# Kernel optimization log

Hardware: AMD Instinct MI355X
Metric: run time of the kernel (lower is better)

Reference implementation:

```python
import jax, jax.numpy as jnp
import numpy as np

B, S, DIM, H = 2, 2048, 2048, 16
HD = DIM // H  # 128
ROPE_THETA = 10000.0
NEG = -1e9


def setup_inputs() -> dict:
    key = jax.random.key(0)
    ks = jax.random.split(key, 6)
    x = jax.random.normal(ks[0], (B, S, DIM), dtype=jnp.float32)
    # rotary embedding tables: angle[s, j] = s / theta^(2j/HD), j in [0, HD/2)
    inv_freq = 1.0 / (ROPE_THETA ** (jnp.arange(0, HD, 2, dtype=jnp.float32) / HD))
    angles = jnp.arange(S, dtype=jnp.float32)[:, None] * inv_freq[None, :]  # (S, HD/2)
    freqs_cos = jnp.cos(angles)
    freqs_sin = jnp.sin(angles)
    # causal additive mask (1,1,S,S)
    causal = jnp.tril(jnp.ones((S, S), dtype=jnp.bool_))
    mask = jnp.where(causal, 0.0, NEG).astype(jnp.float32)[None, None]
    sc = 1.0 / np.sqrt(DIM)
    wq = jax.random.normal(ks[1], (DIM, DIM), dtype=jnp.float32) * sc
    wk = jax.random.normal(ks[2], (DIM, DIM), dtype=jnp.float32) * sc
    wv = jax.random.normal(ks[3], (DIM, DIM), dtype=jnp.float32) * sc
    wo = jax.random.normal(ks[4], (DIM, DIM), dtype=jnp.float32) * sc
    return {"x": x, "freqs_cos": freqs_cos, "freqs_sin": freqs_sin,
            "mask": mask, "wq": wq, "wk": wk, "wv": wv, "wo": wo}


def _apply_rope(t, cos, sin):
    # t: (B,S,H,HD); cos/sin: (S, HD/2) -> broadcast (1,S,1,HD/2)
    tr = t[..., ::2]
    ti = t[..., 1::2]
    c = cos[None, :, None, :]
    s = sin[None, :, None, :]
    out_r = tr * c - ti * s
    out_i = tr * s + ti * c
    # interleave back: stack on last axis then flatten -> [r0,i0,r1,i1,...]
    return jnp.stack([out_r, out_i], axis=-1).reshape(t.shape)


def reference(x, freqs_cos, freqs_sin, mask, wq, wk, wv, wo):
    b, s, _ = x.shape
    xq = (x @ wq).reshape(b, s, H, HD)
    xk = (x @ wk).reshape(b, s, H, HD)
    xv = (x @ wv).reshape(b, s, H, HD)
    xq = _apply_rope(xq, freqs_cos, freqs_sin)
    xk = _apply_rope(xk, freqs_cos, freqs_sin)
    # (B,H,S,HD)
    q = jnp.transpose(xq, (0, 2, 1, 3)) * (1.0 / np.sqrt(HD))
    k = jnp.transpose(xk, (0, 2, 1, 3))
    v = jnp.transpose(xv, (0, 2, 1, 3))
    attn = jnp.einsum('bhqd,bhkd->bhqk', q, k) + mask[:, :, :s, :s]
    attn = jax.nn.softmax(attn, axis=-1)
    out = jnp.einsum('bhqk,bhkd->bhqd', attn, v)  # (B,H,S,HD)
    out = jnp.transpose(out, (0, 2, 1, 3)).reshape(b, s, H * HD)
    return out @ wo
```

## Files before the change

### kernel.cpp

```cpp
#include <hip/hip_runtime.h>
#include <hip/hip_bf16.h>
#include <cstdint>
#include <cstddef>

#define BB   2
#define SS   2048
#define DD   2048
#define HH   16
#define HDD  128
#define SEC  8388608
#define NKT  32

typedef unsigned short u16;
typedef __attribute__((ext_vector_type(8))) short short8;
typedef __attribute__((ext_vector_type(4))) float f32x4;

__device__ __forceinline__ u16 f2bf(float f) {
  union { float f; uint32_t u; } v; v.f = f;
  uint32_t r = v.u + 0x7fffu + ((v.u >> 16) & 1u);
  return (u16)(r >> 16);
}
__device__ __forceinline__ float bf2f(u16 b) {
  union { uint32_t u; float f; } v; v.u = ((uint32_t)b) << 16;
  return v.f;
}

__device__ __forceinline__ void gload16(const u16* g, u16* l) {
  __builtin_amdgcn_global_load_lds(
      (__attribute__((address_space(1))) void*)g,
      (__attribute__((address_space(3))) void*)l, 16, 0, 0);
}

__global__ void k_prep(const float* __restrict__ x,
                       const float* __restrict__ w0, const float* __restrict__ w1,
                       const float* __restrict__ w2, const float* __restrict__ w3,
                       u16* __restrict__ xb, u16* __restrict__ wt) {
  const int z = blockIdx.z;
  if (z == 4) {
    const int id = blockIdx.y * 64 + blockIdx.x;
    const int t = threadIdx.y * 32 + threadIdx.x;
    const size_t base = ((size_t)id * 256 + t) * 2;
    const float4* xv = reinterpret_cast<const float4*>(x);
    uint2* ov = reinterpret_cast<uint2*>(xb);
#pragma unroll
    for (int u = 0; u < 2; ++u) {
      const float4 v = xv[base + u];
      uint2 p;
      p.x = (uint32_t)f2bf(v.x) | ((uint32_t)f2bf(v.y) << 16);
      p.y = (uint32_t)f2bf(v.z) | ((uint32_t)f2bf(v.w) << 16);
      ov[base + u] = p;
    }
    return;
  }
  __shared__ float tls[32][33];
  const float* w = (z == 0) ? w0 : (z == 1) ? w1 : (z == 2) ? w2 : w3;
  u16* o = wt + (size_t)z * (DD * DD);
  const int n0 = blockIdx.x * 32, k0 = blockIdx.y * 32;
  const int tx = threadIdx.x, ty = threadIdx.y;
#pragma unroll
  for (int i = 0; i < 32; i += 8)
    tls[ty + i][tx] = w[(size_t)(k0 + ty + i) * DD + n0 + tx];
  __syncthreads();
#pragma unroll
  for (int i = 0; i < 32; i += 8)
    o[(size_t)(n0 + ty + i) * DD + k0 + tx] = f2bf(tls[tx][ty + i]);
}

__global__ __launch_bounds__(512, 2) void k_qkv(const u16* __restrict__ A,
                                                const u16* __restrict__ Bt,
                                                u16* __restrict__ out,
                                                const float* __restrict__ fc,
                                                const float* __restrict__ fs) {
  __shared__ __align__(16) u16 As[2][2][128 * 64];
  __shared__ __align__(16) u16 Bs[2][2][128 * 64];
  const int tid = threadIdx.x;
  const int wave = tid >> 6, lane = tid & 63;
  const int c = lane & 15, g = lane >> 4;
  const int wm = wave >> 2, wn = wave & 3;
  const int x7 = c & 7;
  const int lb = blockIdx.x;
  const int wg = (lb & 7) * 48 + (lb >> 3);
  const int bx = wg / 24, by = wg % 24;
  const int row0 = bx * 256, col0 = by * 256;
  const int lr3 = lane >> 3;
  const int kch = ((lane & 7) ^ lr3) << 3;

  auto stgA = [&](int t, int h) {
    u16* dst = &As[t & 1][h][0];
#pragma unroll
    for (int u = 0; u < 2; ++u)
      gload16(A + (size_t)(row0 + u * 128 + h * 64 + wave * 8 + lr3) * DD + t * 64 + kch,
              dst + (u * 64 + wave * 8) * 64);
  };
  auto stgB = [&](int t, int h) {
    u16* dst = &Bs[t & 1][h][0];
#pragma unroll
    for (int u = 0; u < 2; ++u)
      gload16(Bt + (size_t)(col0 + u * 128 + wm * 64 + h * 32 + wn * 8 + lr3) * DD + t * 64 + kch,
              dst + (u * 64 + wave * 8) * 64);
  };
  auto rdA = [&](const u16* bp, int ip, int ks) {
    return *reinterpret_cast<const short8*>(
        bp + (wm * 64 + ip * 16 + c) * 64 + ((((ks << 2) | g) ^ x7) << 3));
  };
  auto rdB = [&](const u16* bp, int jp, int ks) {
    return *reinterpret_cast<const short8*>(
        bp + (wn * 32 + jp * 16 + c) * 64 + ((((ks << 2) | g) ^ x7) << 3));
  };

  f32x4 acc[8][4] = {};
  auto quad = [&](short8 (&af)[4][2], short8 (&bf)[2][2], int io, int jo) {
    __builtin_amdgcn_s_setprio(1);
#pragma unroll
    for (int ks = 0; ks < 2; ++ks)
#pragma unroll
      for (int ip = 0; ip < 4; ++ip)
#pragma unroll
        for (int jp = 0; jp < 2; ++jp)
          acc[io + ip][jo + jp] = __builtin_amdgcn_mfma_f32_16x16x32_bf16(
              af[ip][ks], bf[jp][ks], acc[io + ip][jo + jp], 0, 0, 0);
    __builtin_amdgcn_s_setprio(0);
  };
  auto bar = [&]() {
    asm volatile("" ::: "memory");
    __builtin_amdgcn_s_barrier();
    asm volatile("" ::: "memory");
  };

  stgA(0, 0); stgB(0, 0); stgB(0, 1); stgA(0, 1);
  stgA(1, 0); stgB(1, 0); stgB(1, 1); stgA(1, 1);
  asm volatile("s_waitcnt vmcnt(8)" ::: "memory");
  bar();

  short8 a[4][2], b0[2][2], b1[2][2];
  for (int t = 0; t < NKT; ++t) {
    const u16* A0p = &As[t & 1][0][0];
    const u16* A1p = &As[t & 1][1][0];
    const u16* B0p = &Bs[t & 1][0][0];
    const u16* B1p = &Bs[t & 1][1][0];
    const bool pf = (t + 2 < NKT);
#pragma unroll
    for (int ip = 0; ip < 4; ++ip)
#pragma unroll
      for (int ks = 0; ks < 2; ++ks)
        a[ip][ks] = rdA(A0p, ip, ks);
#pragma unroll
    for (int jp = 0; jp < 2; ++jp)
#pragma unroll
      for (int ks = 0; ks < 2; ++ks)
        b0[jp][ks] = rdB(B0p, jp, ks);
    quad(a, b0, 0, 0);
    bar();
#pragma unroll
    for (int jp = 0; jp < 2; ++jp)
#pragma unroll
      for (int ks = 0; ks < 2; ++ks)
        b1[jp][ks] = rdB(B1p, jp, ks);
    if (pf) { stgA(t + 2, 0); stgB(t + 2, 0); }
    quad(a, b1, 0, 2);
    bar();
#pragma unroll
    for (int ip = 0; ip < 4; ++ip)
#pragma unroll
      for (int ks = 0; ks < 2; ++ks)
        a[ip][ks] = rdA(A1p, ip, ks);
    if (pf) stgB(t + 2, 1);
    quad(a, b0, 4, 0);
    bar();
    if (pf) stgA(t + 2, 1);
    if (t < NKT - 2)
      asm volatile("s_waitcnt vmcnt(8)" ::: "memory");
    else if (t == NKT - 2)
      asm volatile("s_waitcnt vmcnt(0)" ::: "memory");
    quad(a, b1, 4, 2);
    bar();
  }

  const int which = col0 >> 11;
#pragma unroll
  for (int i = 0; i < 8; ++i) {
    const int mb = row0 + wm * 128 + i * 16 + g * 4;
    const int b_ = mb >> 11, s0_ = mb & (SS - 1);
#pragma unroll
    for (int j = 0; j < 4; ++j) {
      const int n = col0 + wn * 64 + j * 16 + c;
      const int h_ = (n >> 7) & 15, d_ = n & (HDD - 1);
      if (which == 2) {
        ushort4 pk;
        pk.x = f2bf(acc[i][j][0]); pk.y = f2bf(acc[i][j][1]);
        pk.z = f2bf(acc[i][j][2]); pk.w = f2bf(acc[i][j][3]);
        *reinterpret_cast<ushort4*>(
            out + 2 * (size_t)SEC + (((size_t)(b_ * HH + h_)) * HDD + d_) * SS + s0_) = pk;
      } else {
        const int p = d_ >> 1;
        const bool ev = (d_ & 1) == 0;
        const float qsc = (which == 0) ? 0.08838834764831845f : 1.0f;
#pragma unroll
        for (int r = 0; r < 4; ++r) {
          const int s_ = s0_ + r;
          const float own = acc[i][j][r];
          const float par = __shfl_xor(own, 1);
          const float cv = fc[s_ * 64 + p], sv = fs[s_ * 64 + p];
          const float ro = ev ? (own * cv - par * sv) : (par * sv + own * cv);
          out[(size_t)which * SEC + (((size_t)(b_ * HH + h_)) * SS + s_) * HDD + d_] =
              f2bf(ro * qsc);
        }
      }
    }
  }
}

template <int MODE>
__global__ __launch_bounds__(256) void k_gemm(const u16* __restrict__ A,
                                              const u16* __restrict__ Bt,
                                              void* __restrict__ out,
                                              const float* __restrict__ fc,
                                              const float* __restrict__ fs) {
  __shared__ __align__(16) u16 As[128 * 32];
  __shared__ __align__(16) u16 Bs[128 * 32];
  const int tid = threadIdx.x;
  const int wave = tid >> 6, lane = tid & 63;
  const int c = lane & 15, g = lane >> 4;
  const int row0 = blockIdx.x * 128, col0 = blockIdx.y * 128;
  const int wm = wave >> 1, wn = wave & 1;
  const int sr = lane >> 2;
  const int sk = (lane & 3) * 8;
  f32x4 acc[4][4] = {};
  for (int k0 = 0; k0 < DD; k0 += 32) {
#pragma unroll
    for (int r = 0; r < 2; ++r) {
      const int chunk = r * 4 + wave;
      const int row = chunk * 16 + sr;
      gload16(A  + (size_t)(row0 + row) * DD + k0 + sk, As + chunk * 512);
      gload16(Bt + (size_t)(col0 + row) * DD + k0 + sk, Bs + chunk * 512);
    }
    __syncthreads();
    short8 a[4], b[4];
#pragma unroll
    for (int i = 0; i < 4; ++i)
      a[i] = *reinterpret_cast<const short8*>(As + (wm * 64 + i * 16 + c) * 32 + g * 8);
#pragma unroll
    for (int j = 0; j < 4; ++j)
      b[j] = *reinterpret_cast<const short8*>(Bs + (wn * 64 + j * 16 + c) * 32 + g * 8);
#pragma unroll
    for (int i = 0; i < 4; ++i)
#pragma unroll
      for (int j = 0; j < 4; ++j)
        acc[i][j] = __builtin_amdgcn_mfma_f32_16x16x32_bf16(a[i], b[j], acc[i][j], 0, 0, 0);
    __syncthreads();
  }
#pragma unroll
  for (int i = 0; i < 4; ++i) {
#pragma unroll
    for (int j = 0; j < 4; ++j) {
      const int mb = row0 + wm * 64 + i * 16 + g * 4;
      const int n  = col0 + wn * 64 + j * 16 + c;
#pragma unroll
      for (int r = 0; r < 4; ++r)
        reinterpret_cast<float*>(out)[(size_t)(mb + r) * DD + n] = acc[i][j][r];
    }
  }
}

__global__ __launch_bounds__(256, 3) void k_attn(const u16* __restrict__ Q,
                                                 const u16* __restrict__ K,
                                                 const u16* __restrict__ Vt,
                                                 u16* __restrict__ O) {
  __shared__ __align__(16) u16 Kt[2][32 * 128];
  __shared__ __align__(16) u16 Vs[2][128 * 32];
  __shared__ __align__(16) u16 Pb[4 * 32 * 40];
  const int tid = threadIdx.x;
  const int wave = tid >> 6, lane = tid & 63;
  const int c = lane & 15, g = lane >> 4;
  const int l = blockIdx.x;
  int qi, bh;
  if (l < 256) { qi = 8 + (l & 7); bh = l >> 3; }
  else         { qi = 7 - ((l - 256) & 7); bh = (l - 256) >> 3; }
  const int q0 = qi * 128;
  const u16* Qp = Q  + (size_t)bh * SS * HDD;
  const u16* Kp = K  + (size_t)bh * SS * HDD;
  const u16* Vp = Vt + (size_t)bh * SS * HDD;
  short8 qf[2][4];
#pragma unroll
  for (int ms = 0; ms < 2; ++ms)
#pragma unroll
    for (int kd = 0; kd < 4; ++kd)
      qf[ms][kd] = *reinterpret_cast<const short8*>(
          Qp + (size_t)(q0 + wave * 32 + ms * 16 + c) * HDD + kd * 32 + g * 8);
  f32x4 acc[2][8] = {};
  float psum[2][4] = {};
  const int ntiles = (qi + 1) * 4;
  u16* pwav = Pb + wave * (32 * 40);
  const int krl = lane >> 4, kcl = lane & 15;
  const int vrl = lane >> 2, vcl = lane & 3;
  auto stage = [&](int t) {
    const int kv0 = t * 32;
    u16* kb = Kt[t & 1];
    u16* vb = Vs[t & 1];
#pragma unroll
    for (int j = 0; j < 2; ++j) {
      const int r0k = (j * 4 + wave) * 4;
      const int rowk = r0k + krl;
      gload16(Kp + (size_t)(kv0 + rowk) * HDD + ((kcl ^ (rowk & 15)) << 3),
              kb + r0k * 128);
      const int r0v = (j * 4 + wave) * 16;
      const int rowv = r0v + vrl;
      gload16(Vp + (size_t)rowv * SS + kv0 + ((vcl ^ (vrl & 3)) << 3),
              vb + r0v * 32);
    }
  };
  stage(0);
  for (int t = 0; t < ntiles; ++t) {
    __syncthreads();
    if (t + 1 < ntiles) stage(t + 1);
    const int kv0 = t * 32;
    const bool active = kv0 <= q0 + wave * 32 + 31;
    if (!active) continue;
    const u16* kb = Kt[t & 1];
    const u16* vv = Vs[t & 1];
    f32x4 s[2][2] = {};
#pragma unroll
    for (int ns = 0; ns < 2; ++ns)
#pragma unroll
      for (int kd = 0; kd < 4; ++kd) {
        const short8 b = *reinterpret_cast<const short8*>(
            kb + (ns * 16 + c) * 128 + (((kd * 4 + g) ^ c) << 3));
        s[0][ns] = __builtin_amdgcn_mfma_f32_16x16x32_bf16(qf[0][kd], b, s[0][ns], 0, 0, 0);
        s[1][ns] = __builtin_amdgcn_mfma_f32_16x16x32_bf16(qf[1][kd], b, s[1][ns], 0, 0, 0);
      }
#pragma unroll
    for (int ms = 0; ms < 2; ++ms) {
      const int qrow = q0 + wave * 32 + ms * 16 + g * 4;
#pragma unroll
      for (int r = 0; r < 4; ++r) {
        u16* pw = pwav + (ms * 16 + g * 4 + r) * 40 + c;
        float rs = 0.f;
#pragma unroll
        for (int ns = 0; ns < 2; ++ns) {
          const bool u = (kv0 + ns * 16 + c) <= (qrow + r);
          const float p = u ? __expf(s[ms][ns][r]) : 0.f;
          rs += p;
          pw[ns * 16] = f2bf(p);
        }
        psum[ms][r] += rs;
      }
    }
    short8 pa[2];
    pa[0] = *reinterpret_cast<const short8*>(pwav + c * 40 + g * 8);
    pa[1] = *reinterpret_cast<const short8*>(pwav + (16 + c) * 40 + g * 8);
#pragma unroll
    for (int nb = 0; nb < 8; ++nb) {
      const short8 vb2 = *reinterpret_cast<const short8*>(
          vv + (nb * 16 + c) * 32 + ((g ^ (c & 3)) << 3));
      acc[0][nb] = __builtin_amdgcn_mfma_f32_16x16x32_bf16(pa[0], vb2, acc[0][nb], 0, 0, 0);
      acc[1][nb] = __builtin_amdgcn_mfma_f32_16x16x32_bf16(pa[1], vb2, acc[1][nb], 0, 0, 0);
    }
  }
  const int b_ = bh >> 4, h_ = bh & 15;
#pragma unroll
  for (int ms = 0; ms < 2; ++ms) {
#pragma unroll
    for (int r = 0; r < 4; ++r) {
      float rs = psum[ms][r];
      rs += __shfl_xor(rs, 1);
      rs += __shfl_xor(rs, 2);
      rs += __shfl_xor(rs, 4);
      rs += __shfl_xor(rs, 8);
      const float inv = 1.f / rs;
      const int s_ = q0 + wave * 32 + ms * 16 + g * 4 + r;
      u16* op = O + ((size_t)(b_ * SS + s_)) * DD + h_ * HDD;
#pragma unroll
      for (int nb = 0; nb < 8; ++nb)
        op[nb * 16 + c] = f2bf(acc[ms][nb][r] * inv);
    }
  }
}

extern "C" void kernel_launch(void* const* d_in, const int* in_sizes, int n_in,
                              void* d_out, int out_size, void* d_ws, size_t ws_size,
                              hipStream_t stream) {
  const float* x  = (const float*)d_in[0];
  const float* fc = (const float*)d_in[1];
  const float* fs = (const float*)d_in[2];
  const float* wq = (const float*)d_in[4];
  const float* wk = (const float*)d_in[5];
  const float* wv = (const float*)d_in[6];
  const float* wo = (const float*)d_in[7];

  u16* ws  = (u16*)d_ws;
  u16* xb  = ws;
  u16* wqt = xb  + 8388608;
  u16* wot = wqt + 3 * 4194304;
  u16* Qb  = wot + 4194304;
  u16* Kb  = Qb  + SEC;
  u16* Vtb = Kb  + SEC;
  u16* ao  = Vtb + SEC;

  k_prep<<<dim3(64, 64, 5), dim3(32, 8), 0, stream>>>(x, wq, wk, wv, wo, xb, wqt);
  k_qkv<<<384, 512, 0, stream>>>(xb, wqt, Qb, fc, fs);
  k_attn<<<512, 256, 0, stream>>>(Qb, Kb, Vtb, ao);
  k_gemm<1><<<dim3(32, 16), 256, 0, stream>>>(ao, wot, d_out, nullptr, nullptr);
}
```

Baseline: 415.6 us.

## Load K/V fragments directly from global memory in attention, dropping LDS staging

Removes the double-buffered shared-memory staging of K and V tiles and the per-tile block barrier in the attention kernel. Each wave now reads its K and V MFMA operands straight from global memory and runs only as many KV tiles as its own causal extent needs. This removes barrier stalls and idle waves, but every wave now fetches K/V separately (four times the global/L2 traffic). Loads are no longer prefetched, so latency is exposed.

Result: slower. 478.2 us (+15.1%).

```diff
diff --git a/kernel.cpp b/kernel.cpp
--- a/kernel.cpp
+++ b/kernel.cpp
@@ -266,8 +266,6 @@
                                                  const u16* __restrict__ K,
                                                  const u16* __restrict__ Vt,
                                                  u16* __restrict__ O) {
-  __shared__ __align__(16) u16 Kt[2][32 * 128];
-  __shared__ __align__(16) u16 Vs[2][128 * 32];
   __shared__ __align__(16) u16 Pb[4 * 32 * 40];
   const int tid = threadIdx.x;
   const int wave = tid >> 6, lane = tid & 63;
@@ -289,42 +287,17 @@
           Qp + (size_t)(q0 + wave * 32 + ms * 16 + c) * HDD + kd * 32 + g * 8);
   f32x4 acc[2][8] = {};
   float psum[2][4] = {};
-  const int ntiles = (qi + 1) * 4;
   u16* pwav = Pb + wave * (32 * 40);
-  const int krl = lane >> 4, kcl = lane & 15;
-  const int vrl = lane >> 2, vcl = lane & 3;
-  auto stage = [&](int t) {
+  const int mytiles = qi * 4 + wave + 1;
+  for (int t = 0; t < mytiles; ++t) {
     const int kv0 = t * 32;
-    u16* kb = Kt[t & 1];
-    u16* vb = Vs[t & 1];
-#pragma unroll
-    for (int j = 0; j < 2; ++j) {
-      const int r0k = (j * 4 + wave) * 4;
-      const int rowk = r0k + krl;
-      gload16(Kp + (size_t)(kv0 + rowk) * HDD + ((kcl ^ (rowk & 15)) << 3),
-              kb + r0k * 128);
-      const int r0v = (j * 4 + wave) * 16;
-      const int rowv = r0v + vrl;
-      gload16(Vp + (size_t)rowv * SS + kv0 + ((vcl ^ (vrl & 3)) << 3),
-              vb + r0v * 32);
-    }
-  };
-  stage(0);
-  for (int t = 0; t < ntiles; ++t) {
-    __syncthreads();
-    if (t + 1 < ntiles) stage(t + 1);
-    const int kv0 = t * 32;
-    const bool active = kv0 <= q0 + wave * 32 + 31;
-    if (!active) continue;
-    const u16* kb = Kt[t & 1];
-    const u16* vv = Vs[t & 1];
     f32x4 s[2][2] = {};
 #pragma unroll
     for (int ns = 0; ns < 2; ++ns)
 #pragma unroll
       for (int kd = 0; kd < 4; ++kd) {
         const short8 b = *reinterpret_cast<const short8*>(
-            kb + (ns * 16 + c) * 128 + (((kd * 4 + g) ^ c) << 3));
+            Kp + (size_t)(kv0 + ns * 16 + c) * HDD + kd * 32 + g * 8);
         s[0][ns] = __builtin_amdgcn_mfma_f32_16x16x32_bf16(qf[0][kd], b, s[0][ns], 0, 0, 0);
         s[1][ns] = __builtin_amdgcn_mfma_f32_16x16x32_bf16(qf[1][kd], b, s[1][ns], 0, 0, 0);
       }
@@ -351,7 +324,7 @@
 #pragma unroll
     for (int nb = 0; nb < 8; ++nb) {
       const short8 vb2 = *reinterpret_cast<const short8*>(
-          vv + (nb * 16 + c) * 32 + ((g ^ (c & 3)) << 3));
+          Vp + (size_t)(nb * 16 + c) * SS + kv0 + g * 8);
       acc[0][nb] = __builtin_amdgcn_mfma_f32_16x16x32_bf16(pa[0], vb2, acc[0][nb], 0, 0, 0);
       acc[1][nb] = __builtin_amdgcn_mfma_f32_16x16x32_bf16(pa[1], vb2, acc[1][nb], 0, 0, 0);
     }
```

## Replace output projection GEMM with double-buffered swizzled 256x128 pipelined kernel

Applied to the files above, without the earlier changes.

Replaces the simple single-buffered output-projection GEMM with a new kernel, k_out. It uses 512 threads, 256x128 tiles and a K-step of 64, with LDS double-buffered so the next tiles' global loads overlap with the current tile's MFMAs. The A tile is split into two halves with staggered loads and explicit vmcnt waits, LDS reads use XOR swizzling to avoid bank conflicts, and block IDs are remapped to group tiles across XCDs. This aims to remove load-latency stalls and barrier serialisation, at the cost of more LDS per block and fragile hand-tuned wait counts.

Measured after the change: 425.8 us. 1.02x slower.

```diff
diff --git a/kernel.cpp b/kernel.cpp
--- a/kernel.cpp
+++ b/kernel.cpp
@@ -210,54 +210,118 @@
   }
 }
 
-template <int MODE>
-__global__ __launch_bounds__(256) void k_gemm(const u16* __restrict__ A,
-                                              const u16* __restrict__ Bt,
-                                              void* __restrict__ out,
-                                              const float* __restrict__ fc,
-                                              const float* __restrict__ fs) {
-  __shared__ __align__(16) u16 As[128 * 32];
-  __shared__ __align__(16) u16 Bs[128 * 32];
+__global__ __launch_bounds__(512, 2) void k_out(const u16* __restrict__ A,
+                                                const u16* __restrict__ Bt,
+                                                float* __restrict__ out) {
+  __shared__ __align__(16) u16 As[2][2][128 * 64];
+  __shared__ __align__(16) u16 Bs[2][128 * 64];
   const int tid = threadIdx.x;
   const int wave = tid >> 6, lane = tid & 63;
   const int c = lane & 15, g = lane >> 4;
-  const int row0 = blockIdx.x * 128, col0 = blockIdx.y * 128;
-  const int wm = wave >> 1, wn = wave & 1;
-  const int sr = lane >> 2;
-  const int sk = (lane & 3) * 8;
-  f32x4 acc[4][4] = {};
-  for (int k0 = 0; k0 < DD; k0 += 32) {
-#pragma unroll
-    for (int r = 0; r < 2; ++r) {
-      const int chunk = r * 4 + wave;
-      const int row = chunk * 16 + sr;
-      gload16(A  + (size_t)(row0 + row) * DD + k0 + sk, As + chunk * 512);
-      gload16(Bt + (size_t)(col0 + row) * DD + k0 + sk, Bs + chunk * 512);
-    }
-    __syncthreads();
-    short8 a[4], b[4];
-#pragma unroll
-    for (int i = 0; i < 4; ++i)
-      a[i] = *reinterpret_cast<const short8*>(As + (wm * 64 + i * 16 + c) * 32 + g * 8);
-#pragma unroll
-    for (int j = 0; j < 4; ++j)
-      b[j] = *reinterpret_cast<const short8*>(Bs + (wn * 64 + j * 16 + c) * 32 + g * 8);
-#pragma unroll
-    for (int i = 0; i < 4; ++i)
-#pragma unroll
-      for (int j = 0; j < 4; ++j)
-        acc[i][j] = __builtin_amdgcn_mfma_f32_16x16x32_bf16(a[i], b[j], acc[i][j], 0, 0, 0);
-    __syncthreads();
-  }
-#pragma unroll
-  for (int i = 0; i < 4; ++i) {
-#pragma unroll
-    for (int j = 0; j < 4; ++j) {
-      const int mb = row0 + wm * 64 + i * 16 + g * 4;
-      const int n  = col0 + wn * 64 + j * 16 + c;
+  const int wm = wave >> 2, wn = wave & 3;
+  const int x7 = c & 7;
+  const int lb = blockIdx.x;
+  const int wg = (lb & 7) * 32 + (lb >> 3);
+  const int bx = wg >> 4, by = wg & 15;
+  const int row0 = bx * 256, col0 = by * 128;
+  const int lr3 = lane >> 3;
+  const int kch = ((lane & 7) ^ lr3) << 3;
+
+  auto stgA = [&](int t, int h) {
+    u16* dst = &As[t & 1][h][0];
+#pragma unroll
+    for (int u = 0; u < 2; ++u)
+      gload16(A + (size_t)(row0 + u * 128 + h * 64 + wave * 8 + lr3) * DD + t * 64 + kch,
+              dst + (u * 64 + wave * 8) * 64);
+  };
+  auto stgB = [&](int t) {
+    u16* dst = &Bs[t & 1][0];
+#pragma unroll
+    for (int u = 0; u < 2; ++u) {
+      const int r0 = u * 64 + wave * 8;
+      gload16(Bt + (size_t)(col0 + r0 + lr3) * DD + t * 64 + kch,
+              dst + r0 * 64);
+    }
+  };
+  auto rdA = [&](const u16* bp, int ip, int ks) {
+    return *reinterpret_cast<const short8*>(
+        bp + (wm * 64 + ip * 16 + c) * 64 + ((((ks << 2) | g) ^ x7) << 3));
+  };
+  auto rdB = [&](const u16* bp, int jp, int ks) {
+    return *reinterpret_cast<const short8*>(
+        bp + (wn * 32 + jp * 16 + c) * 64 + ((((ks << 2) | g) ^ x7) << 3));
+  };
+
+  f32x4 acc[8][2] = {};
+  auto quad = [&](short8 (&af)[4][2], short8 (&bf)[2][2], int io) {
+    __builtin_amdgcn_s_setprio(1);
+#pragma unroll
+    for (int ks = 0; ks < 2; ++ks)
+#pragma unroll
+      for (int ip = 0; ip < 4; ++ip)
+#pragma unroll
+        for (int jp = 0; jp < 2; ++jp)
+          acc[io + ip][jp] = __builtin_amdgcn_mfma_f32_16x16x32_bf16(
+              af[ip][ks], bf[jp][ks], acc[io + ip][jp], 0, 0, 0);
+    __builtin_amdgcn_s_setprio(0);
+  };
+  auto bar = [&]() {
+    asm volatile("" ::: "memory");
+    __builtin_amdgcn_s_barrier();
+    asm volatile("" ::: "memory");
+  };
+
+  stgA(0, 0); stgB(0);
+  stgA(0, 1);
+  stgA(1, 0); stgB(1);
+  asm volatile("s_waitcnt vmcnt(6)" ::: "memory");
+  bar();
+
+  short8 a[4][2], b[2][2];
+  for (int t = 0; t < NKT; ++t) {
+    const u16* A0p = &As[t & 1][0][0];
+    const u16* A1p = &As[t & 1][1][0];
+    const u16* Bp  = &Bs[t & 1][0];
+    if (t + 1 < NKT) stgA(t + 1, 1);
+#pragma unroll
+    for (int ip = 0; ip < 4; ++ip)
+#pragma unroll
+      for (int ks = 0; ks < 2; ++ks)
+        a[ip][ks] = rdA(A0p, ip, ks);
+#pragma unroll
+    for (int jp = 0; jp < 2; ++jp)
+#pragma unroll
+      for (int ks = 0; ks < 2; ++ks)
+        b[jp][ks] = rdB(Bp, jp, ks);
+    quad(a, b, 0);
+    if (t < NKT - 1)
+      asm volatile("s_waitcnt vmcnt(6)" ::: "memory");
+    else
+      asm volatile("s_waitcnt vmcnt(0)" ::: "memory");
+    bar();
+    if (t + 2 < NKT) { stgA(t + 2, 0); stgB(t + 2); }
+#pragma unroll
+    for (int ip = 0; ip < 4; ++ip)
+#pragma unroll
+      for (int ks = 0; ks < 2; ++ks)
+        a[ip][ks] = rdA(A1p, ip, ks);
+    quad(a, b, 4);
+    if (t < NKT - 2)
+      asm volatile("s_waitcnt vmcnt(6)" ::: "memory");
+    else if (t == NKT - 2)
+      asm volatile("s_waitcnt vmcnt(2)" ::: "memory");
+    bar();
+  }
+
+#pragma unroll
+  for (int i = 0; i < 8; ++i) {
+    const int mb = row0 + wm * 128 + i * 16 + g * 4;
+#pragma unroll
+    for (int j = 0; j < 2; ++j) {
+      const int n = col0 + wn * 32 + j * 16 + c;
 #pragma unroll
       for (int r = 0; r < 4; ++r)
-        reinterpret_cast<float*>(out)[(size_t)(mb + r) * DD + n] = acc[i][j][r];
+        out[(size_t)(mb + r) * DD + n] = acc[i][j][r];
     }
   }
 }
@@ -399,5 +463,5 @@
   k_prep<<<dim3(64, 64, 5), dim3(32, 8), 0, stream>>>(x, wq, wk, wv, wo, xb, wqt);
   k_qkv<<<384, 512, 0, stream>>>(xb, wqt, Qb, fc, fs);
   k_attn<<<512, 256, 0, stream>>>(Qb, Kb, Vtb, ao);
-  k_gemm<1><<<dim3(32, 16), 256, 0, stream>>>(ao, wot, d_out, nullptr, nullptr);
-}
+  k_out<<<256, 512, 0, stream>>>(ao, wot, (float*)d_out);
+}
```
